# Performance work log

Measured on AMD Instinct MI355X. Metric: run time of the kernel, lower is better.

The kernel has to match this reference:

```python
import jax, jax.numpy as jnp
import numpy as np

N_NODES = 50000
N_EDGES = 600000
D = 128
EPS = 1e-5


def setup_inputs() -> dict:
    key = jax.random.key(0)
    ks = jax.random.split(key, 12)
    s = 1.0 / np.sqrt(D)
    return {
        "h": jax.random.normal(ks[0], (N_NODES, D), dtype=jnp.float32),
        "src": jax.random.randint(ks[1], (N_EDGES,), 0, N_NODES),
        "dst": jax.random.randint(ks[2], (N_EDGES,), 0, N_NODES),
        "W_pre": jax.random.uniform(ks[3], (D, D), jnp.float32, -s, s),
        "b_pre": jax.random.uniform(ks[4], (D,), jnp.float32, -s, s),
        "W1": jax.random.uniform(ks[5], (D, D), jnp.float32, -s, s),
        "b1": jax.random.uniform(ks[6], (D,), jnp.float32, -s, s),
        "W2": jax.random.uniform(ks[7], (D, D), jnp.float32, -s, s),
        "b2": jax.random.uniform(ks[8], (D,), jnp.float32, -s, s),
        "gamma": jnp.ones((D,), jnp.float32),
        "beta": jnp.zeros((D,), jnp.float32),
    }


def layer_norm(x, gamma, beta):
    mu = jnp.mean(x, axis=-1, keepdims=True)
    var = jnp.mean(jnp.square(x - mu), axis=-1, keepdims=True)
    return (x - mu) * jax.lax.rsqrt(var + EPS) * gamma + beta


def reference(h, src, dst, W_pre, b_pre, W1, b1, W2, b2, gamma, beta):
    # pre-projection: [N, D]
    h = h @ W_pre + b_pre
    # message passing: gather from src, segment-sum at dst (copy_u + sum)
    agg = jax.ops.segment_sum(h[src], dst, num_segments=N_NODES)
    # MLP (dropout is identity in eval)
    h_new = jax.nn.relu(jax.nn.relu(agg @ W1 + b1) @ W2 + b2)
    # residual + LayerNorm
    return layer_norm(h + h_new, gamma, beta)
```

## Files before the change

kernel.cpp:

```cpp
#include <hip/hip_runtime.h>

#define D 128
#define EPS 1e-5f
#define SCAN_CHUNK 1024
#define TSTRIDE 136

typedef __attribute__((ext_vector_type(8))) short bf16x8;
typedef __attribute__((ext_vector_type(4))) float floatx4;

__device__ __forceinline__ unsigned short f2bf(float f) {
    union { float f; unsigned u; } v; v.f = f;
    unsigned r = v.u + 0x7fffu + ((v.u >> 16) & 1u);
    return (unsigned short)(r >> 16);
}
__device__ __forceinline__ float bf2f(unsigned short s) {
    union { unsigned u; float f; } v; v.u = ((unsigned)s) << 16; return v.f;
}

__global__ __launch_bounds__(256) void prep(const float* __restrict__ W0,
                                            const float* __restrict__ W1,
                                            const float* __restrict__ W2,
                                            unsigned short* __restrict__ wt,
                                            int* __restrict__ counts, int nN) {
    int idx = blockIdx.x * 256 + threadIdx.x;
    if (idx < 3 * D * D) {
        int w = idx >> 14;
        int r = idx & (D * D - 1);
        int f = r >> 7, k = r & (D - 1);
        const float* W = (w == 0) ? W0 : (w == 1) ? W1 : W2;
        wt[(size_t)w * D * D + (size_t)f * D + k] = f2bf(W[(size_t)k * D + f]);
    }
    if (idx < nN) counts[idx] = 0;
}

__global__ __launch_bounds__(256) void hist_dst(const int* __restrict__ dst,
                                                int* __restrict__ counts, int nE) {
    int e = blockIdx.x * 256 + threadIdx.x;
    if (e < nE) atomicAdd(&counts[dst[e]], 1);
}

__global__ __launch_bounds__(256) void scan_chunk_sums(const int* __restrict__ counts,
                                                       int* __restrict__ chunkSums, int n) {
    __shared__ int sh[256];
    const int t = threadIdx.x;
    const int base = blockIdx.x * SCAN_CHUNK + t * 4;
    int s = 0;
#pragma unroll
    for (int i = 0; i < 4; ++i) {
        int idx = base + i;
        if (idx < n) s += counts[idx];
    }
    sh[t] = s;
    __syncthreads();
    for (int off = 128; off > 0; off >>= 1) {
        if (t < off) sh[t] += sh[t + off];
        __syncthreads();
    }
    if (t == 0) chunkSums[blockIdx.x] = sh[0];
}

__global__ __launch_bounds__(64) void scan_top(int* __restrict__ chunkSums, int nChunks,
                                               int* __restrict__ offsets, int nN, int nE) {
    const int t = threadIdx.x;
    int orig = (t < nChunks) ? chunkSums[t] : 0;
    int v = orig;
#pragma unroll
    for (int off = 1; off < 64; off <<= 1) {
        int u = __shfl_up(v, off, 64);
        if (t >= off) v += u;
    }
    if (t < nChunks) chunkSums[t] = v - orig;
    if (t == 0) offsets[nN] = nE;
}

__global__ __launch_bounds__(256) void scan_final(const int* __restrict__ counts,
                                                  const int* __restrict__ chunkSums,
                                                  int* __restrict__ offsets,
                                                  int* __restrict__ cursor, int n) {
    __shared__ int sh[256];
    const int t = threadIdx.x;
    const int base = blockIdx.x * SCAN_CHUNK + t * 4;
    int c[4];
    int s = 0;
#pragma unroll
    for (int i = 0; i < 4; ++i) {
        int idx = base + i;
        c[i] = (idx < n) ? counts[idx] : 0;
        s += c[i];
    }
    sh[t] = s;
    __syncthreads();
    int val = s;
    for (int off = 1; off < 256; off <<= 1) {
        int u = (t >= off) ? sh[t - off] : 0;
        __syncthreads();
        val += u;
        sh[t] = val;
        __syncthreads();
    }
    int run = val - s + chunkSums[blockIdx.x];
#pragma unroll
    for (int i = 0; i < 4; ++i) {
        int idx = base + i;
        if (idx < n) {
            offsets[idx] = run;
            cursor[idx] = run;
        }
        run += c[i];
    }
}

__global__ __launch_bounds__(256) void fill_edges(const int* __restrict__ src,
                                                  const int* __restrict__ dst,
                                                  int* __restrict__ cursor,
                                                  int* __restrict__ edge_src, int nE) {
    int e = blockIdx.x * 256 + threadIdx.x;
    if (e < nE) {
        int pos = atomicAdd(&cursor[dst[e]], 1);
        edge_src[pos] = src[e];
    }
}

__global__ __launch_bounds__(256) void gemm1(const float* __restrict__ X,
                                             const unsigned short* __restrict__ Wt,
                                             const float* __restrict__ bias,
                                             unsigned short* __restrict__ Y, int nrows) {
    const int t = threadIdx.x;
    const int lane = t & 63, wave = t >> 6;
    const int ml = lane & 15, q = lane >> 4;
    const int node = blockIdx.x * 64 + wave * 16 + ml;
    const int rr = (node < nrows) ? node : (nrows - 1);
    const bool ok = (node < nrows);

    bf16x8 bfrag[4];
    const float* xp = X + (size_t)rr * D + q * 8;
#pragma unroll
    for (int kb = 0; kb < 4; ++kb) {
        float4 f0 = *(const float4*)(xp + kb * 32);
        float4 f1 = *(const float4*)(xp + kb * 32 + 4);
        bf16x8 v;
        v[0] = (short)f2bf(f0.x); v[1] = (short)f2bf(f0.y);
        v[2] = (short)f2bf(f0.z); v[3] = (short)f2bf(f0.w);
        v[4] = (short)f2bf(f1.x); v[5] = (short)f2bf(f1.y);
        v[6] = (short)f2bf(f1.z); v[7] = (short)f2bf(f1.w);
        bfrag[kb] = v;
    }

#pragma unroll
    for (int tl = 0; tl < 8; ++tl) {
        floatx4 acc = {0.f, 0.f, 0.f, 0.f};
        const unsigned short* wp = Wt + (size_t)(tl * 16 + ml) * D + q * 8;
#pragma unroll
        for (int kb = 0; kb < 4; ++kb) {
            bf16x8 af = *(const bf16x8*)(wp + kb * 32);
            acc = __builtin_amdgcn_mfma_f32_16x16x32_bf16(af, bfrag[kb], acc, 0, 0, 0);
        }
        const int f0i = tl * 16 + q * 4;
        float4 b4 = *(const float4*)(bias + f0i);
        if (ok) {
            ushort4 o;
            o.x = f2bf(acc[0] + b4.x); o.y = f2bf(acc[1] + b4.y);
            o.z = f2bf(acc[2] + b4.z); o.w = f2bf(acc[3] + b4.w);
            *(ushort4*)(Y + (size_t)node * D + f0i) = o;
        }
    }
}

__global__ __launch_bounds__(256) void gather_sum(const unsigned short* __restrict__ hpre,
                                                  const int* __restrict__ offsets,
                                                  const int* __restrict__ edge_src,
                                                  unsigned short* __restrict__ agg, int nN) {
    const int t = threadIdx.x;
    const int li = t & 15;
    const int n = blockIdx.x * 16 + (t >> 4);
    if (n >= nN) return;
    const int beg = offsets[n], end = offsets[n + 1];

    float a[8] = {0.f, 0.f, 0.f, 0.f, 0.f, 0.f, 0.f, 0.f};
    int j = beg;
    int s0 = 0, s1 = 0;
    if (j < end) s0 = edge_src[j];
    if (j + 1 < end) s1 = edge_src[j + 1];

    while (j + 1 < end) {
        const int c0 = s0, c1 = s1;
        const int jn = j + 2;
        if (jn < end) s0 = edge_src[jn];
        if (jn + 1 < end) s1 = edge_src[jn + 1];
        bf16x8 v0 = *(const bf16x8*)(hpre + (size_t)c0 * D + li * 8);
        bf16x8 v1 = *(const bf16x8*)(hpre + (size_t)c1 * D + li * 8);
#pragma unroll
        for (int i = 0; i < 8; ++i)
            a[i] += bf2f((unsigned short)v0[i]) + bf2f((unsigned short)v1[i]);
        j = jn;
    }
    if (j < end) {
        bf16x8 v0 = *(const bf16x8*)(hpre + (size_t)s0 * D + li * 8);
#pragma unroll
        for (int i = 0; i < 8; ++i) a[i] += bf2f((unsigned short)v0[i]);
    }

    bf16x8 p;
#pragma unroll
    for (int i = 0; i < 8; ++i) p[i] = (short)f2bf(a[i]);
    *(bf16x8*)(agg + (size_t)n * D + li * 8) = p;
}

__global__ __launch_bounds__(256) void fused_mlp(const unsigned short* __restrict__ agg,
                                                 const unsigned short* __restrict__ hpre,
                                                 const unsigned short* __restrict__ Wt1,
                                                 const float* __restrict__ b1,
                                                 const unsigned short* __restrict__ Wt2,
                                                 const float* __restrict__ b2,
                                                 const float* __restrict__ gamma,
                                                 const float* __restrict__ beta,
                                                 float* __restrict__ out, int nN) {
    __shared__ unsigned short tile[64 * TSTRIDE];
    const int t = threadIdx.x;
    const int wave = t >> 6, lane = t & 63;
    const int ml = lane & 15, q = lane >> 4;
    const int row = wave * 16 + ml;
    const int node = blockIdx.x * 64 + row;
    const int rr = (node < nN) ? node : (nN - 1);
    const bool ok = (node < nN);

    {
        bf16x8 bfrag[4];
        const unsigned short* xp = agg + (size_t)rr * D + q * 8;
#pragma unroll
        for (int kb = 0; kb < 4; ++kb) bfrag[kb] = *(const bf16x8*)(xp + kb * 32);

        float accs[8][4];
#pragma unroll
        for (int tl = 0; tl < 8; ++tl) {
            floatx4 acc = {0.f, 0.f, 0.f, 0.f};
            const unsigned short* wp = Wt1 + (size_t)(tl * 16 + ml) * D + q * 8;
#pragma unroll
            for (int kb = 0; kb < 4; ++kb) {
                bf16x8 af = *(const bf16x8*)(wp + kb * 32);
                acc = __builtin_amdgcn_mfma_f32_16x16x32_bf16(af, bfrag[kb], acc, 0, 0, 0);
            }
            const int f0i = tl * 16 + q * 4;
            float4 b4 = *(const float4*)(b1 + f0i);
            accs[tl][0] = fmaxf(acc[0] + b4.x, 0.f);
            accs[tl][1] = fmaxf(acc[1] + b4.y, 0.f);
            accs[tl][2] = fmaxf(acc[2] + b4.z, 0.f);
            accs[tl][3] = fmaxf(acc[3] + b4.w, 0.f);
        }
#pragma unroll
        for (int tl = 0; tl < 8; ++tl) {
            ushort4 o;
            o.x = f2bf(accs[tl][0]); o.y = f2bf(accs[tl][1]);
            o.z = f2bf(accs[tl][2]); o.w = f2bf(accs[tl][3]);
            *(ushort4*)(&tile[row * TSTRIDE + tl * 16 + q * 4]) = o;
        }
    }
    __syncthreads();

    {
        bf16x8 bfrag[4];
#pragma unroll
        for (int kb = 0; kb < 4; ++kb)
            bfrag[kb] = *(const bf16x8*)(&tile[row * TSTRIDE + kb * 32 + q * 8]);

        float vs[8][4];
        float sm = 0.f, sq = 0.f;
#pragma unroll
        for (int tl = 0; tl < 8; ++tl) {
            floatx4 acc = {0.f, 0.f, 0.f, 0.f};
            const unsigned short* wp = Wt2 + (size_t)(tl * 16 + ml) * D + q * 8;
#pragma unroll
            for (int kb = 0; kb < 4; ++kb) {
                bf16x8 af = *(const bf16x8*)(wp + kb * 32);
                acc = __builtin_amdgcn_mfma_f32_16x16x32_bf16(af, bfrag[kb], acc, 0, 0, 0);
            }
            const int f0i = tl * 16 + q * 4;
            float4 b4 = *(const float4*)(b2 + f0i);
            ushort4 hr = ((const ushort4*)(hpre + (size_t)rr * D + f0i))[0];
            float a0 = fmaxf(acc[0] + b4.x, 0.f) + bf2f(hr.x);
            float a1 = fmaxf(acc[1] + b4.y, 0.f) + bf2f(hr.y);
            float a2 = fmaxf(acc[2] + b4.z, 0.f) + bf2f(hr.z);
            float a3 = fmaxf(acc[3] + b4.w, 0.f) + bf2f(hr.w);
            vs[tl][0] = a0; vs[tl][1] = a1; vs[tl][2] = a2; vs[tl][3] = a3;
            sm += a0 + a1 + a2 + a3;
            sq += a0 * a0 + a1 * a1 + a2 * a2 + a3 * a3;
        }

        sm += __shfl_xor(sm, 16); sm += __shfl_xor(sm, 32);
        sq += __shfl_xor(sq, 16); sq += __shfl_xor(sq, 32);

        const float mu = sm * (1.f / D);
        const float var = sq * (1.f / D) - mu * mu;
        const float is = rsqrtf(var + EPS);

        if (ok) {
#pragma unroll
            for (int tl = 0; tl < 8; ++tl) {
                const int f0i = tl * 16 + q * 4;
                float4 g4 = *(const float4*)(gamma + f0i);
                float4 be4 = *(const float4*)(beta + f0i);
                float4 o;
                o.x = (vs[tl][0] - mu) * is * g4.x + be4.x;
                o.y = (vs[tl][1] - mu) * is * g4.y + be4.y;
                o.z = (vs[tl][2] - mu) * is * g4.z + be4.z;
                o.w = (vs[tl][3] - mu) * is * g4.w + be4.w;
                *(float4*)(out + (size_t)node * D + f0i) = o;
            }
        }
    }
}

extern "C" void kernel_launch(void* const* d_in, const int* in_sizes, int n_in,
                              void* d_out, int out_size, void* d_ws, size_t ws_size,
                              hipStream_t stream) {
    const float* h     = (const float*)d_in[0];
    const int*   src   = (const int*)d_in[1];
    const int*   dst   = (const int*)d_in[2];
    const float* W_pre = (const float*)d_in[3];
    const float* b_pre = (const float*)d_in[4];
    const float* W1    = (const float*)d_in[5];
    const float* b1    = (const float*)d_in[6];
    const float* W2    = (const float*)d_in[7];
    const float* b2    = (const float*)d_in[8];
    const float* gamma = (const float*)d_in[9];
    const float* beta  = (const float*)d_in[10];
    float* out = (float*)d_out;

    const int nN = in_sizes[0] / D;
    const int nE = in_sizes[1];
    const size_t rowsz = (size_t)nN * D;

    unsigned short* hpre = (unsigned short*)d_ws;
    unsigned short* agg  = hpre + rowsz;
    unsigned short* wt   = agg + rowsz;
    int* edge_src  = (int*)(wt + 3 * D * D);
    int* offsets   = edge_src + nE;
    int* cursor    = offsets + nN + 1;
    int* counts    = cursor + nN;
    int* chunkSums = counts + nN;

    const int prep_n  = (3 * D * D > nN) ? 3 * D * D : nN;
    const int eblocks = (nE + 255) / 256;
    const int gblocks = (nN + 63) / 64;
    const int nChunks = (nN + SCAN_CHUNK - 1) / SCAN_CHUNK;

    prep<<<(prep_n + 255) / 256, 256, 0, stream>>>(W_pre, W1, W2, wt, counts, nN);
    hist_dst<<<eblocks, 256, 0, stream>>>(dst, counts, nE);
    scan_chunk_sums<<<nChunks, 256, 0, stream>>>(counts, chunkSums, nN);
    scan_top<<<1, 64, 0, stream>>>(chunkSums, nChunks, offsets, nN, nE);
    scan_final<<<nChunks, 256, 0, stream>>>(counts, chunkSums, offsets, cursor, nN);
    fill_edges<<<eblocks, 256, 0, stream>>>(src, dst, cursor, edge_src, nE);

    gemm1<<<gblocks, 256, 0, stream>>>(h, wt, b_pre, hpre, nN);
    gather_sum<<<(nN + 15) / 16, 256, 0, stream>>>(hpre, offsets, edge_src, agg, nN);
    fused_mlp<<<gblocks, 256, 0, stream>>>(agg, hpre, wt + D * D, b1, wt + 2 * D * D, b2,
                                           gamma, beta, out, nN);
}
```

Measured before the change: 243.9 us.

## Split output columns across wave pairs in gemm1 and fused MLP

Each block now handles 32 nodes instead of 64, with pairs of waves sharing a 16-row group and each wave computing half of the 128 output features. Per-thread work and register use drop, and the grid doubles to raise occupancy and parallelism. LayerNorm statistics are combined across the two half-waves through shared memory, which adds an extra barrier. Each wave also reloads the same input fragments, duplicating some input reads.

```diff
diff --git a/kernel.cpp b/kernel.cpp
--- a/kernel.cpp
+++ b/kernel.cpp
@@ -127,8 +127,9 @@
                                              unsigned short* __restrict__ Y, int nrows) {
     const int t = threadIdx.x;
     const int lane = t & 63, wave = t >> 6;
+    const int g = wave >> 1, hf = wave & 1;
     const int ml = lane & 15, q = lane >> 4;
-    const int node = blockIdx.x * 64 + wave * 16 + ml;
+    const int node = blockIdx.x * 32 + g * 16 + ml;
     const int rr = (node < nrows) ? node : (nrows - 1);
     const bool ok = (node < nrows);
 
@@ -147,7 +148,8 @@
     }
 
 #pragma unroll
-    for (int tl = 0; tl < 8; ++tl) {
+    for (int tl2 = 0; tl2 < 4; ++tl2) {
+        const int tl = hf * 4 + tl2;
         floatx4 acc = {0.f, 0.f, 0.f, 0.f};
         const unsigned short* wp = Wt + (size_t)(tl * 16 + ml) * D + q * 8;
 #pragma unroll
@@ -215,12 +217,14 @@
                                                  const float* __restrict__ gamma,
                                                  const float* __restrict__ beta,
                                                  float* __restrict__ out, int nN) {
-    __shared__ unsigned short tile[64 * TSTRIDE];
-    const int t = threadIdx.x;
-    const int wave = t >> 6, lane = t & 63;
+    __shared__ unsigned short tile[32 * TSTRIDE];
+    __shared__ float psm[2][32], psq[2][32];
+    const int t = threadIdx.x;
+    const int lane = t & 63, wave = t >> 6;
+    const int g = wave >> 1, hf = wave & 1;
     const int ml = lane & 15, q = lane >> 4;
-    const int row = wave * 16 + ml;
-    const int node = blockIdx.x * 64 + row;
+    const int lr = g * 16 + ml;
+    const int node = blockIdx.x * 32 + lr;
     const int rr = (node < nN) ? node : (nN - 1);
     const bool ok = (node < nN);
 
@@ -230,9 +234,9 @@
 #pragma unroll
         for (int kb = 0; kb < 4; ++kb) bfrag[kb] = *(const bf16x8*)(xp + kb * 32);
 
-        float accs[8][4];
-#pragma unroll
-        for (int tl = 0; tl < 8; ++tl) {
+#pragma unroll
+        for (int tl2 = 0; tl2 < 4; ++tl2) {
+            const int tl = hf * 4 + tl2;
             floatx4 acc = {0.f, 0.f, 0.f, 0.f};
             const unsigned short* wp = Wt1 + (size_t)(tl * 16 + ml) * D + q * 8;
 #pragma unroll
@@ -242,31 +246,27 @@
             }
             const int f0i = tl * 16 + q * 4;
             float4 b4 = *(const float4*)(b1 + f0i);
-            accs[tl][0] = fmaxf(acc[0] + b4.x, 0.f);
-            accs[tl][1] = fmaxf(acc[1] + b4.y, 0.f);
-            accs[tl][2] = fmaxf(acc[2] + b4.z, 0.f);
-            accs[tl][3] = fmaxf(acc[3] + b4.w, 0.f);
-        }
-#pragma unroll
-        for (int tl = 0; tl < 8; ++tl) {
             ushort4 o;
-            o.x = f2bf(accs[tl][0]); o.y = f2bf(accs[tl][1]);
-            o.z = f2bf(accs[tl][2]); o.w = f2bf(accs[tl][3]);
-            *(ushort4*)(&tile[row * TSTRIDE + tl * 16 + q * 4]) = o;
+            o.x = f2bf(fmaxf(acc[0] + b4.x, 0.f));
+            o.y = f2bf(fmaxf(acc[1] + b4.y, 0.f));
+            o.z = f2bf(fmaxf(acc[2] + b4.z, 0.f));
+            o.w = f2bf(fmaxf(acc[3] + b4.w, 0.f));
+            *(ushort4*)(&tile[lr * TSTRIDE + f0i]) = o;
         }
     }
     __syncthreads();
 
+    float vs[4][4];
+    float sm = 0.f, sq = 0.f;
     {
         bf16x8 bfrag[4];
 #pragma unroll
         for (int kb = 0; kb < 4; ++kb)
-            bfrag[kb] = *(const bf16x8*)(&tile[row * TSTRIDE + kb * 32 + q * 8]);
-
-        float vs[8][4];
-        float sm = 0.f, sq = 0.f;
-#pragma unroll
-        for (int tl = 0; tl < 8; ++tl) {
+            bfrag[kb] = *(const bf16x8*)(&tile[lr * TSTRIDE + kb * 32 + q * 8]);
+
+#pragma unroll
+        for (int tl2 = 0; tl2 < 4; ++tl2) {
+            const int tl = hf * 4 + tl2;
             floatx4 acc = {0.f, 0.f, 0.f, 0.f};
             const unsigned short* wp = Wt2 + (size_t)(tl * 16 + ml) * D + q * 8;
 #pragma unroll
@@ -281,29 +281,34 @@
             float a1 = fmaxf(acc[1] + b4.y, 0.f) + bf2f(hr.y);
             float a2 = fmaxf(acc[2] + b4.z, 0.f) + bf2f(hr.z);
             float a3 = fmaxf(acc[3] + b4.w, 0.f) + bf2f(hr.w);
-            vs[tl][0] = a0; vs[tl][1] = a1; vs[tl][2] = a2; vs[tl][3] = a3;
+            vs[tl2][0] = a0; vs[tl2][1] = a1; vs[tl2][2] = a2; vs[tl2][3] = a3;
             sm += a0 + a1 + a2 + a3;
             sq += a0 * a0 + a1 * a1 + a2 * a2 + a3 * a3;
         }
-
         sm += __shfl_xor(sm, 16); sm += __shfl_xor(sm, 32);
         sq += __shfl_xor(sq, 16); sq += __shfl_xor(sq, 32);
-
-        const float mu = sm * (1.f / D);
-        const float var = sq * (1.f / D) - mu * mu;
+        if (lane < 16) { psm[hf][lr] = sm; psq[hf][lr] = sq; }
+    }
+    __syncthreads();
+
+    {
+        const float smT = psm[0][lr] + psm[1][lr];
+        const float sqT = psq[0][lr] + psq[1][lr];
+        const float mu = smT * (1.f / D);
+        const float var = sqT * (1.f / D) - mu * mu;
         const float is = rsqrtf(var + EPS);
 
         if (ok) {
 #pragma unroll
-            for (int tl = 0; tl < 8; ++tl) {
-                const int f0i = tl * 16 + q * 4;
+            for (int tl2 = 0; tl2 < 4; ++tl2) {
+                const int f0i = (hf * 4 + tl2) * 16 + q * 4;
                 float4 g4 = *(const float4*)(gamma + f0i);
                 float4 be4 = *(const float4*)(beta + f0i);
                 float4 o;
-                o.x = (vs[tl][0] - mu) * is * g4.x + be4.x;
-                o.y = (vs[tl][1] - mu) * is * g4.y + be4.y;
-                o.z = (vs[tl][2] - mu) * is * g4.z + be4.z;
-                o.w = (vs[tl][3] - mu) * is * g4.w + be4.w;
+                o.x = (vs[tl2][0] - mu) * is * g4.x + be4.x;
+                o.y = (vs[tl2][1] - mu) * is * g4.y + be4.y;
+                o.z = (vs[tl2][2] - mu) * is * g4.z + be4.z;
+                o.w = (vs[tl2][3] - mu) * is * g4.w + be4.w;
                 *(float4*)(out + (size_t)node * D + f0i) = o;
             }
         }
@@ -341,7 +346,7 @@
 
     const int prep_n  = (3 * D * D > nN) ? 3 * D * D : nN;
     const int eblocks = (nE + 255) / 256;
-    const int gblocks = (nN + 63) / 64;
+    const int gblocks = (nN + 31) / 32;
     const int nChunks = (nN + SCAN_CHUNK - 1) / SCAN_CHUNK;
 
     prep<<<(prep_n + 255) / 256, 256, 0, stream>>>(W_pre, W1, W2, wt, counts, nN);
```

Measured after the change: 243.3 us. No clear change (-0.2%).
